# Performance work log

Hardware: AMD Instinct MI355X
Metric: run time of the kernel (lower is better)

Reference implementation:

```python
import jax, jax.numpy as jnp
import numpy as np

N = 50000      # nodes
E = 800000     # edges (before self-loops)
IN = 128       # in_channels
HID = 32       # hidden_channels
H = 4          # heads (hidden layers)
H_LAST = 6     # heads of final conv (concat=False -> mean)
OUT = 2        # out_channels
NEG = 0.2      # LeakyReLU slope in GATConv


def setup_inputs() -> dict:
    key = jax.random.key(0)
    ks = jax.random.split(key, 24)
    r = lambda k, s, sc=0.1: (jax.random.normal(k, s, jnp.float32) * sc)
    inp = {
        "x": jax.random.normal(ks[0], (N, IN), jnp.float32),
        "edge_index": jax.random.randint(ks[1], (2, E), 0, N, dtype=jnp.int32),
        "edge_attr": jax.random.normal(ks[2], (E, 1), jnp.float32),  # ignored by GATConv (edge_dim=None)
        # layer 0: GATConv(IN -> HID, heads=H, concat) + Linear(IN -> HID*H)
        "c0_W": r(ks[3], (IN, H * HID)), "c0_as": r(ks[4], (H, HID)), "c0_ad": r(ks[5], (H, HID)), "c0_b": jnp.zeros((H * HID,), jnp.float32),
        "l0_W": r(ks[6], (IN, H * HID)), "l0_b": jnp.zeros((H * HID,), jnp.float32),
        # layer 1 (middle): GATConv(HID*H -> HID, heads=H) + Linear(HID*H -> HID*H)
        "c1_W": r(ks[7], (H * HID, H * HID)), "c1_as": r(ks[8], (H, HID)), "c1_ad": r(ks[9], (H, HID)), "c1_b": jnp.zeros((H * HID,), jnp.float32),
        "l1_W": r(ks[10], (H * HID, H * HID)), "l1_b": jnp.zeros((H * HID,), jnp.float32),
        # layer 2 (last): GATConv(HID*H -> OUT, heads=H_LAST, concat=False) + Linear(HID*H -> OUT)
        "c2_W": r(ks[11], (H * HID, H_LAST * OUT)), "c2_as": r(ks[12], (H_LAST, OUT)), "c2_ad": r(ks[13], (H_LAST, OUT)), "c2_b": jnp.zeros((OUT,), jnp.float32),
        "l2_W": r(ks[14], (H * HID, OUT)), "l2_b": jnp.zeros((OUT,), jnp.float32),
    }
    return inp


def gat_conv(x, src, dst, W, a_src, a_dst, b, heads, ch, concat):
    n = x.shape[0]
    xw = (x @ W).reshape(n, heads, ch)                      # [N,H,C]
    al_s = jnp.einsum('nhc,hc->nh', xw, a_src)              # [N,H]
    al_d = jnp.einsum('nhc,hc->nh', xw, a_dst)
    alpha = jax.nn.leaky_relu(al_s[src] + al_d[dst], NEG)   # [E,H]
    # segment softmax over edges sharing the same destination node
    m = jax.ops.segment_max(alpha, dst, num_segments=n)
    e = jnp.exp(alpha - m[dst])
    s = jax.ops.segment_sum(e, dst, num_segments=n)
    coef = e / s[dst]                                       # [E,H]
    out = jax.ops.segment_sum(xw[src] * coef[:, :, None], dst, num_segments=n)  # [N,H,C]
    out = out.reshape(n, heads * ch) if concat else out.mean(axis=1)
    return out + b


def reference(x, edge_index, edge_attr,
              c0_W, c0_as, c0_ad, c0_b, l0_W, l0_b,
              c1_W, c1_as, c1_ad, c1_b, l1_W, l1_b,
              c2_W, c2_as, c2_ad, c2_b, l2_W, l2_b):
    n = x.shape[0]
    loops = jnp.arange(n, dtype=edge_index.dtype)  # GATConv add_self_loops=True
    src = jnp.concatenate([edge_index[0], loops])
    dst = jnp.concatenate([edge_index[1], loops])
    # edge_attr is ignored: GATConv built without edge_dim has lin_edge=None
    h = jax.nn.relu(gat_conv(x, src, dst, c0_W, c0_as, c0_ad, c0_b, H, HID, True) + x @ l0_W + l0_b)
    h = jax.nn.relu(gat_conv(h, src, dst, c1_W, c1_as, c1_ad, c1_b, H, HID, True) + h @ l1_W + l1_b)
    out = gat_conv(h, src, dst, c2_W, c2_as, c2_ad, c2_b, H_LAST, OUT, False) + h @ l2_W + l2_b
    return out
```

## Files before the change

kernel.cpp:

```cpp
#include <hip/hip_runtime.h>
#include <hip/hip_bf16.h>


#define NEG_SLOPE 0.2f
#define SC_CHUNK 4096
#define CAP 64
#define XCROWS 16

typedef __attribute__((ext_vector_type(8))) short short8;
typedef __attribute__((ext_vector_type(4))) float floatx4;

static __device__ __forceinline__ float leaky(float x) {
    return x > 0.f ? x : NEG_SLOPE * x;
}

static __device__ __forceinline__ unsigned short f2bf(float f) {
    unsigned int u = __float_as_uint(f);
    u = (u + 0x7fffu + ((u >> 16) & 1u)) >> 16;
    return (unsigned short)u;
}

static __device__ __forceinline__ unsigned int pack_bf2(float lo, float hi) {
    return (unsigned int)f2bf(lo) | ((unsigned int)f2bf(hi) << 16);
}

static __device__ __forceinline__ float bflo(unsigned int u) {
    return __uint_as_float(u << 16);
}
static __device__ __forceinline__ float bfhi(unsigned int u) {
    return __uint_as_float(u & 0xffff0000u);
}

__global__ __launch_bounds__(256) void k_bucket(
    const int* __restrict__ ei, int E, int N, int rs, int chunks,
    int* __restrict__ cnt, unsigned short* __restrict__ col,
    const float* __restrict__ W0, unsigned short* __restrict__ T0,
    const float* __restrict__ W1, unsigned short* __restrict__ T1,
    const float* __restrict__ W2, unsigned short* __restrict__ T2,
    const float* __restrict__ W3, unsigned short* __restrict__ T3,
    const float* __restrict__ c2W, const float* __restrict__ l2W,
    unsigned short* __restrict__ WT5,
    const float* __restrict__ x, unsigned short* __restrict__ Ab0, int Mpad) {
    int y = blockIdx.y;
    if (y == chunks) {
        int tid = blockIdx.x * 256 + threadIdx.x;
        for (int j = tid; j < 65536; j += 2048) {
            int wsel = j >> 14, t = j & 16383;
            int n = t >> 7, k = t & 127;
            const float* W = (wsel == 0) ? W0 : (wsel == 1) ? W1 : (wsel == 2) ? W2 : W3;
            unsigned short* T = (wsel == 0) ? T0 : (wsel == 1) ? T1 : (wsel == 2) ? T2 : T3;
            T[n * 128 + k] = f2bf(W[k * 128 + n]);
        }
        {
            int n = tid >> 7, k = tid & 127;
            float v = 0.f;
            if (n < 12) v = c2W[k * 12 + n];
            else if (n < 14) v = l2W[k * 2 + (n - 12)];
            WT5[n * 128 + k] = f2bf(v);
        }
        return;
    }
    if (y > chunks) {
        int bid = (y - chunks - 1) * 8 + blockIdx.x;
        int tid = bid * 256 + threadIdx.x;
        int total = Mpad * 32;
        int nvalid = N * 32;
        const float4* x4 = (const float4*)x;
        ushort4* o4 = (ushort4*)Ab0;
        for (int i = tid; i < total; i += XCROWS * 8 * 256) {
            ushort4 o;
            if (i < nvalid) {
                float4 v = x4[i];
                o.x = f2bf(v.x); o.y = f2bf(v.y);
                o.z = f2bf(v.z); o.w = f2bf(v.w);
            } else {
                o.x = 0; o.y = 0; o.z = 0; o.w = 0;
            }
            o4[i] = o;
        }
        return;
    }
    int lo = blockIdx.x * rs, hi = lo + rs;
    int base = y * SC_CHUNK;
    int ET = E + N;
#pragma unroll 4
    for (int o = threadIdx.x; o < SC_CHUNK; o += 256) {
        int e = base + o;
        if (e >= ET) break;
        int d = (e < E) ? ei[E + e] : (e - E);
        if (d < lo || d >= hi) continue;
        int s = (e < E) ? ei[e] : d;
        int pos = atomicAdd(&cnt[d], 1);
        if (pos < CAP) col[(d << 6) + pos] = (unsigned short)s;
    }
}

__global__ __launch_bounds__(256) void k_gemm2(
    const unsigned short* __restrict__ Ab,
    const unsigned short* __restrict__ WcT,
    const unsigned short* __restrict__ WlT,
    unsigned int* __restrict__ XWb,
    const float* __restrict__ a_s, const float* __restrict__ a_d,
    float4* __restrict__ ALS4, float4* __restrict__ ALD4,
    const float* __restrict__ lb,
    unsigned short* __restrict__ Hsb,
    int M) {
    __shared__ short8 Wl[128 * 17];
    int w = threadIdx.x >> 6, lane = threadIdx.x & 63;
    int m = lane & 15, q = lane >> 4;
    const short8* A8 = (const short8*)Ab;

    for (int u = threadIdx.x; u < 2048; u += 256)
        Wl[(u >> 4) * 17 + (u & 15)] = ((const short8*)WcT)[u];

    short8 af[2][4];
    int rt0 = blockIdx.x * 8 + w;
#pragma unroll
    for (int t = 0; t < 2; t++) {
        int arow = (rt0 + t * 4) * 16 + m;
#pragma unroll
        for (int ks = 0; ks < 4; ks++)
            af[t][ks] = A8[arow * 16 + ks * 4 + q];
    }
    __syncthreads();

#pragma unroll
    for (int t = 0; t < 2; t++) {
        floatx4 acc[8];
#pragma unroll
        for (int ct = 0; ct < 8; ct++) acc[ct] = (floatx4){0.f, 0.f, 0.f, 0.f};
#pragma unroll
        for (int ks = 0; ks < 4; ks++) {
#pragma unroll
            for (int ct = 0; ct < 8; ct++) {
                short8 bfrag = Wl[(ct * 16 + m) * 17 + ks * 4 + q];
                acc[ct] = __builtin_amdgcn_mfma_f32_16x16x32_bf16(af[t][ks], bfrag, acc[ct], 0, 0, 0);
            }
        }
        int crow0 = (rt0 + t * 4) * 16 + q * 4;
#pragma unroll
        for (int ct = 0; ct < 4; ct++) {
#pragma unroll
            for (int r = 0; r < 4; r++) {
                int gr = crow0 + r;
                if (gr < M)
                    XWb[gr * 64 + ct * 16 + m] = pack_bf2(acc[ct][r], acc[ct + 4][r]);
            }
        }
        float sv[4][4], dv[4][4];
#pragma unroll
        for (int h = 0; h < 4; h++) {
            float as0 = a_s[h * 32 + m], as1 = a_s[h * 32 + 16 + m];
            float ad0 = a_d[h * 32 + m], ad1 = a_d[h * 32 + 16 + m];
#pragma unroll
            for (int r = 0; r < 4; r++) {
                sv[h][r] = acc[2 * h][r] * as0 + acc[2 * h + 1][r] * as1;
                dv[h][r] = acc[2 * h][r] * ad0 + acc[2 * h + 1][r] * ad1;
            }
        }
#pragma unroll
        for (int off = 8; off >= 1; off >>= 1) {
#pragma unroll
            for (int h = 0; h < 4; h++)
#pragma unroll
                for (int r = 0; r < 4; r++) {
                    sv[h][r] += __shfl_xor(sv[h][r], off);
                    dv[h][r] += __shfl_xor(dv[h][r], off);
                }
        }
        if (m == 0) {
#pragma unroll
            for (int r = 0; r < 4; r++) {
                int gr = crow0 + r;
                if (gr < M) {
                    ALS4[gr] = make_float4(sv[0][r], sv[1][r], sv[2][r], sv[3][r]);
                    ALD4[gr] = make_float4(dv[0][r], dv[1][r], dv[2][r], dv[3][r]);
                }
            }
        }
    }

    __syncthreads();
    for (int u = threadIdx.x; u < 2048; u += 256)
        Wl[(u >> 4) * 17 + (u & 15)] = ((const short8*)WlT)[u];
    __syncthreads();

#pragma unroll
    for (int t = 0; t < 2; t++) {
        floatx4 acc[8];
#pragma unroll
        for (int ct = 0; ct < 8; ct++) acc[ct] = (floatx4){0.f, 0.f, 0.f, 0.f};
#pragma unroll
        for (int ks = 0; ks < 4; ks++) {
#pragma unroll
            for (int ct = 0; ct < 8; ct++) {
                short8 bfrag = Wl[(ct * 16 + m) * 17 + ks * 4 + q];
                acc[ct] = __builtin_amdgcn_mfma_f32_16x16x32_bf16(af[t][ks], bfrag, acc[ct], 0, 0, 0);
            }
        }
        int crow0 = (rt0 + t * 4) * 16 + q * 4;
#pragma unroll
        for (int ct = 0; ct < 8; ct++) {
            int gc = ct * 16 + m;
            float bias = lb[gc];
#pragma unroll
            for (int r = 0; r < 4; r++) {
                int gr = crow0 + r;
                if (gr < M) Hsb[gr * 128 + gc] = f2bf(acc[ct][r] + bias);
            }
        }
    }
}

__global__ __launch_bounds__(256) void k_gemm_small(
    const unsigned short* __restrict__ Ab,
    const unsigned short* __restrict__ WT5,
    const float* __restrict__ c2as, const float* __restrict__ c2ad,
    const float* __restrict__ l2b,
    float* __restrict__ L2D, float* __restrict__ ALD2,
    float* __restrict__ out, int M) {
    int w = threadIdx.x >> 6, lane = threadIdx.x & 63;
    int m = lane & 15, q = lane >> 4;
    const short8* A8 = (const short8*)Ab;
    const short8* W8 = (const short8*)WT5;
    floatx4 acc = (floatx4){0.f, 0.f, 0.f, 0.f};
    int arow = blockIdx.x * 64 + w * 16 + m;
#pragma unroll
    for (int ks = 0; ks < 4; ks++) {
        short8 afrag = A8[arow * 16 + ks * 4 + q];
        short8 bfrag = W8[m * 16 + ks * 4 + q];
        acc = __builtin_amdgcn_mfma_f32_16x16x32_bf16(afrag, bfrag, acc, 0, 0, 0);
    }
    float asm_ = (m < 12) ? c2as[m] : 0.f;
    float adm  = (m < 12) ? c2ad[m] : 0.f;
    int crow0 = blockIdx.x * 64 + w * 16 + q * 4;
    float sc[4], dc[4];
#pragma unroll
    for (int r = 0; r < 4; r++) {
        sc[r] = acc[r] * asm_;
        dc[r] = acc[r] * adm;
    }
#pragma unroll
    for (int r = 0; r < 4; r++) {
        sc[r] += __shfl_xor(sc[r], 1);
        dc[r] += __shfl_xor(dc[r], 1);
    }
#pragma unroll
    for (int r = 0; r < 4; r++) {
        int gr = crow0 + r;
        if (gr >= M) continue;
        if (m < 12) {
            L2D[gr * 20 + m] = acc[r];
            if ((m & 1) == 0) {
                int h = m >> 1;
                L2D[gr * 20 + 12 + h] = sc[r];
                ALD2[gr * 8 + h] = dc[r];
            }
        } else if (m == 12) {
            out[gr * 2 + 0] = acc[r] + l2b[0];
        } else if (m == 13) {
            out[gr * 2 + 1] = acc[r] + l2b[1];
        }
    }
}

__global__ __launch_bounds__(256) void k_agg4(
    const int* __restrict__ cntv, const unsigned short* __restrict__ col,
    const uint4* __restrict__ XWb4,
    const float4* __restrict__ ALS4, const float4* __restrict__ ALD4,
    const float* __restrict__ cb,
    const unsigned short* __restrict__ Hsb, unsigned short* __restrict__ Hb, int N) {
    int wid = threadIdx.x >> 6, lane = threadIdx.x & 63;
    int node = blockIdx.x * 4 + wid;
    if (node >= N) return;
    int deg = cntv[node];
    if (deg > CAP) deg = CAP;
    int start = node << 6;
    int gq = lane >> 4, g = lane & 15;
    int hA = g >> 3;
    int cval = col[start + lane];
    float4 cl = ((const float4*)cb)[g];
    float4 ch = ((const float4*)cb)[g + 16];
    uint2 skl = ((const uint2*)(Hsb + node * 128))[g];
    uint2 skh = ((const uint2*)(Hsb + node * 128 + 64))[g];
    float4 ad = ALD4[node];
    float adA = hA ? ad.y : ad.x;
    float adB = hA ? ad.w : ad.z;

    float a0 = 0.f, a1 = 0.f, a2 = 0.f, a3 = 0.f;
    float b0 = 0.f, b1 = 0.f, b2 = 0.f, b3 = 0.f;
    float sA = 0.f, sB = 0.f;

#define QUAD(qq)                                                        \
    bool t##qq; float4 as##qq; uint4 u##qq;                             \
    {                                                                   \
        int idx = (qq) * 4 + gq;                                        \
        t##qq = idx < deg;                                              \
        int sv = __shfl(cval, t##qq ? idx : 0);                         \
        as##qq = ALS4[sv];                                              \
        u##qq = XWb4[(size_t)sv * 16 + g];                              \
    }

#define CQ(qq)                                                          \
    {                                                                   \
        float eA = t##qq ? __expf(leaky((hA ? as##qq.y : as##qq.x) + adA)) : 0.f; \
        float eB = t##qq ? __expf(leaky((hA ? as##qq.w : as##qq.z) + adB)) : 0.f; \
        sA += eA; sB += eB;                                             \
        a0 += eA * bflo(u##qq.x); b0 += eB * bfhi(u##qq.x);             \
        a1 += eA * bflo(u##qq.y); b1 += eB * bfhi(u##qq.y);             \
        a2 += eA * bflo(u##qq.z); b2 += eB * bfhi(u##qq.z);             \
        a3 += eA * bflo(u##qq.w); b3 += eB * bfhi(u##qq.w);             \
    }

    if (deg <= 16) {
        QUAD(0) QUAD(1) QUAD(2) QUAD(3)
        CQ(0) CQ(1) CQ(2) CQ(3)
    } else if (deg <= 24) {
        QUAD(0) QUAD(1) QUAD(2) QUAD(3) QUAD(4) QUAD(5)
        CQ(0) CQ(1) CQ(2) CQ(3) CQ(4) CQ(5)
    } else {
        QUAD(0) QUAD(1) QUAD(2) QUAD(3) QUAD(4) QUAD(5) QUAD(6) QUAD(7)
        CQ(0) CQ(1) CQ(2) CQ(3) CQ(4) CQ(5) CQ(6) CQ(7)
        for (int i = 32; i < deg; i += 4) {
            int idx = i + gq;
            bool tt = idx < deg;
            int sv = __shfl(cval, tt ? idx : 0);
            float4 as = ALS4[sv];
            uint4 uu = XWb4[(size_t)sv * 16 + g];
            float eA = tt ? __expf(leaky((hA ? as.y : as.x) + adA)) : 0.f;
            float eB = tt ? __expf(leaky((hA ? as.w : as.z) + adB)) : 0.f;
            sA += eA; sB += eB;
            a0 += eA * bflo(uu.x); b0 += eB * bfhi(uu.x);
            a1 += eA * bflo(uu.y); b1 += eB * bfhi(uu.y);
            a2 += eA * bflo(uu.z); b2 += eB * bfhi(uu.z);
            a3 += eA * bflo(uu.w); b3 += eB * bfhi(uu.w);
        }
    }
#undef QUAD
#undef CQ

#define RED2(v) { v += __shfl_xor(v, 16); v += __shfl_xor(v, 32); }
    RED2(sA) RED2(sB)
    RED2(a0) RED2(a1) RED2(a2) RED2(a3)
    RED2(b0) RED2(b1) RED2(b2) RED2(b3)
#undef RED2

    if (gq == 0) {
        float invA = 1.f / sA, invB = 1.f / sB;
        float v0 = a0 * invA + cl.x + bflo(skl.x);
        float v1 = a1 * invA + cl.y + bfhi(skl.x);
        float v2 = a2 * invA + cl.z + bflo(skl.y);
        float v3 = a3 * invA + cl.w + bfhi(skl.y);
        float w0 = b0 * invB + ch.x + bflo(skh.x);
        float w1 = b1 * invB + ch.y + bfhi(skh.x);
        float w2 = b2 * invB + ch.z + bflo(skh.y);
        float w3 = b3 * invB + ch.w + bfhi(skh.y);
        v0 = v0 > 0.f ? v0 : 0.f;  v1 = v1 > 0.f ? v1 : 0.f;
        v2 = v2 > 0.f ? v2 : 0.f;  v3 = v3 > 0.f ? v3 : 0.f;
        w0 = w0 > 0.f ? w0 : 0.f;  w1 = w1 > 0.f ? w1 : 0.f;
        w2 = w2 > 0.f ? w2 : 0.f;  w3 = w3 > 0.f ? w3 : 0.f;
        uint2 ol, oh;
        ol.x = pack_bf2(v0, v1); ol.y = pack_bf2(v2, v3);
        oh.x = pack_bf2(w0, w1); oh.y = pack_bf2(w2, w3);
        ((uint2*)(Hb + node * 128))[g] = ol;
        ((uint2*)(Hb + node * 128 + 64))[g] = oh;
    }
}

__global__ __launch_bounds__(256) void k_agg2(
    const int* __restrict__ cntv, const unsigned short* __restrict__ col,
    const float4* __restrict__ L2D4,
    const float* __restrict__ ALD2,
    const float* __restrict__ c2b,
    float* __restrict__ out, int N) {
    int g = threadIdx.x >> 4, l = threadIdx.x & 15;
    int node = blockIdx.x * 16 + g;
    if (node >= N) return;
    int deg = cntv[node];
    if (deg > CAP) deg = CAP;
    int start = node << 6;

    float m0 = (l      < deg) ? 1.f : 0.f;
    float m1 = (l + 16 < deg) ? 1.f : 0.f;
    float m2 = (l + 32 < deg) ? 1.f : 0.f;
    float m3 = (l + 48 < deg) ? 1.f : 0.f;
    int s0 = col[start + ((l      < deg) ? l      : 0)];
    int s1 = col[start + ((l + 16 < deg) ? l + 16 : 0)];
    int s2 = col[start + ((l + 32 < deg) ? l + 32 : 0)];
    int s3 = col[start + ((l + 48 < deg) ? l + 48 : 0)];

    float ald[6];
    {
        float4 d03 = *(const float4*)(ALD2 + node * 8);
        float2 d45 = *(const float2*)(ALD2 + node * 8 + 4);
        ald[0] = d03.x; ald[1] = d03.y; ald[2] = d03.z; ald[3] = d03.w;
        ald[4] = d45.x; ald[5] = d45.y;
    }

#define LOADN(k, sv)                                                       \
    float4 xA##k = L2D4[(size_t)(sv) * 5 + 0];                             \
    float4 xB##k = L2D4[(size_t)(sv) * 5 + 1];                             \
    float4 xC##k = L2D4[(size_t)(sv) * 5 + 2];                             \
    float4 aS##k = L2D4[(size_t)(sv) * 5 + 3];                             \
    float4 aT##k = L2D4[(size_t)(sv) * 5 + 4];
    LOADN(0, s0) LOADN(1, s1) LOADN(2, s2) LOADN(3, s3)
#undef LOADN

    float se[6], a0[6], a1[6];
#pragma unroll
    for (int h = 0; h < 6; h++) { se[h] = 0.f; a0[h] = 0.f; a1[h] = 0.f; }

#define COMPN(k, mk)                                                       \
    {                                                                      \
        float als[6] = {aS##k.x, aS##k.y, aS##k.z, aS##k.w, aT##k.x, aT##k.y}; \
        float xw[12] = {xA##k.x, xA##k.y, xA##k.z, xA##k.w,                \
                        xB##k.x, xB##k.y, xB##k.z, xB##k.w,                \
                        xC##k.x, xC##k.y, xC##k.z, xC##k.w};               \
        _Pragma("unroll")                                                  \
        for (int h = 0; h < 6; h++) {                                      \
            float e = (mk) * __expf(leaky(als[h] + ald[h]));               \
            se[h] += e;                                                    \
            a0[h] += e * xw[2 * h];                                        \
            a1[h] += e * xw[2 * h + 1];                                    \
        }                                                                  \
    }
    COMPN(0, m0) COMPN(1, m1) COMPN(2, m2) COMPN(3, m3)
#undef COMPN

#pragma unroll
    for (int m = 8; m >= 1; m >>= 1) {
#pragma unroll
        for (int h = 0; h < 6; h++) {
            se[h] += __shfl_xor(se[h], m);
            a0[h] += __shfl_xor(a0[h], m);
            a1[h] += __shfl_xor(a1[h], m);
        }
    }
    if (l == 0) {
        float o0 = 0.f, o1 = 0.f;
#pragma unroll
        for (int h = 0; h < 6; h++) {
            float inv = 1.f / se[h];
            o0 += a0[h] * inv;
            o1 += a1[h] * inv;
        }
        out[node * 2 + 0] += o0 * (1.f / 6.f) + c2b[0];
        out[node * 2 + 1] += o1 * (1.f / 6.f) + c2b[1];
    }
}


extern "C" void kernel_launch(void* const* d_in, const int* in_sizes, int n_in,
                              void* d_out, int out_size, void* d_ws, size_t ws_size,
                              hipStream_t stream) {
    const float* x   = (const float*)d_in[0];
    const int* ei    = (const int*)d_in[1];
    const float* c0W = (const float*)d_in[3];
    const float* c0as = (const float*)d_in[4];
    const float* c0ad = (const float*)d_in[5];
    const float* c0b = (const float*)d_in[6];
    const float* l0W = (const float*)d_in[7];
    const float* l0b = (const float*)d_in[8];
    const float* c1W = (const float*)d_in[9];
    const float* c1as = (const float*)d_in[10];
    const float* c1ad = (const float*)d_in[11];
    const float* c1b = (const float*)d_in[12];
    const float* l1W = (const float*)d_in[13];
    const float* l1b = (const float*)d_in[14];
    const float* c2W = (const float*)d_in[15];
    const float* c2as = (const float*)d_in[16];
    const float* c2ad = (const float*)d_in[17];
    const float* c2b = (const float*)d_in[18];
    const float* l2W = (const float*)d_in[19];
    const float* l2b = (const float*)d_in[20];
    float* out = (float*)d_out;

    const int N = in_sizes[0] / 128;
    const int E = in_sizes[1] / 2;
    const int ET = E + N;
    const int Mpad = (N + 63) & ~63;

    char* p = (char*)d_ws;
    auto alloc = [&](size_t bytes) -> void* {
        void* r = (void*)p;
        p += (bytes + 255) & ~(size_t)255;
        return r;
    };
    unsigned short* Hsb = (unsigned short*)alloc((size_t)N * 128 * 2);
    unsigned int* XWb  = (unsigned int*)alloc((size_t)N * 64 * 4);
    unsigned short* Ab0 = (unsigned short*)alloc((size_t)Mpad * 128 * 2);
    unsigned short* AbH = (unsigned short*)alloc((size_t)Mpad * 128 * 2);
    unsigned short* W1T = (unsigned short*)alloc(128 * 128 * 2);
    unsigned short* W2T = (unsigned short*)alloc(128 * 128 * 2);
    unsigned short* W3T = (unsigned short*)alloc(128 * 128 * 2);
    unsigned short* W4T = (unsigned short*)alloc(128 * 128 * 2);
    unsigned short* WT5 = (unsigned short*)alloc(16 * 128 * 2);
    float* ALS = (float*)alloc((size_t)N * 4 * 4);
    float* ALD = (float*)alloc((size_t)N * 8 * 4);
    float* L2D = (float*)alloc((size_t)N * 20 * 4);
    int* cnt    = (int*)alloc((size_t)N * 4);
    unsigned short* col = (unsigned short*)alloc((size_t)N * CAP * 2);

    hipMemsetAsync(cnt, 0, (size_t)N * 4, stream);
    int rs = (N + 7) / 8;
    int chunks = (ET + SC_CHUNK - 1) / SC_CHUNK;
    dim3 bgrid(8, chunks + 1 + XCROWS);
    k_bucket<<<bgrid, 256, 0, stream>>>(ei, E, N, rs, chunks, cnt, col,
                                        c0W, W1T, l0W, W2T, c1W, W3T, l1W, W4T,
                                        c2W, l2W, WT5, x, Ab0, Mpad);

    int gx = (Mpad + 127) / 128;
    int nwb = (N + 3) / 4;

    k_gemm2<<<gx, 256, 0, stream>>>(Ab0, W1T, W2T, XWb, c0as, c0ad,
                                    (float4*)ALS, (float4*)ALD, l0b, Hsb, N);
    k_agg4<<<nwb, 256, 0, stream>>>(cnt, col, (const uint4*)XWb,
                                    (const float4*)ALS, (const float4*)ALD,
                                    c0b, Hsb, AbH, N);

    k_gemm2<<<gx, 256, 0, stream>>>(AbH, W3T, W4T, XWb, c1as, c1ad,
                                    (float4*)ALS, (float4*)ALD, l1b, Hsb, N);
    k_agg4<<<nwb, 256, 0, stream>>>(cnt, col, (const uint4*)XWb,
                                    (const float4*)ALS, (const float4*)ALD,
                                    c1b, Hsb, Ab0, N);

    k_gemm_small<<<Mpad / 64, 256, 0, stream>>>(Ab0, WT5, c2as, c2ad, l2b,
                                                L2D, ALD, out, N);
    k_agg2<<<(N + 15) / 16, 256, 0, stream>>>(cnt, col, (const float4*)L2D,
                                              ALD, c2b, out, N);
}
```

Measured before the change: 297.5 us.

## Fuse final small GEMM into layer-1 aggregation kernel

Merges the last-layer projection (128->14 GEMM plus the attention logits) into the second aggregation kernel. The projection becomes an FP32 dot product against weights staged in shared memory, followed by a shuffle reduction. This removes one kernel launch and the round trip of the bf16 hidden activations through global memory. In exchange, every block rebuilds the weight table in LDS and runs extra shuffles, and the separate per-layer ALD buffers are split so the two layers no longer alias.

Result: slower. 308.3 us (+3.6%).

```diff
diff --git a/kernel.cpp b/kernel.cpp
--- a/kernel.cpp
+++ b/kernel.cpp
@@ -208,58 +208,6 @@
                 int gr = crow0 + r;
                 if (gr < M) Hsb[gr * 128 + gc] = f2bf(acc[ct][r] + bias);
             }
-        }
-    }
-}
-
-__global__ __launch_bounds__(256) void k_gemm_small(
-    const unsigned short* __restrict__ Ab,
-    const unsigned short* __restrict__ WT5,
-    const float* __restrict__ c2as, const float* __restrict__ c2ad,
-    const float* __restrict__ l2b,
-    float* __restrict__ L2D, float* __restrict__ ALD2,
-    float* __restrict__ out, int M) {
-    int w = threadIdx.x >> 6, lane = threadIdx.x & 63;
-    int m = lane & 15, q = lane >> 4;
-    const short8* A8 = (const short8*)Ab;
-    const short8* W8 = (const short8*)WT5;
-    floatx4 acc = (floatx4){0.f, 0.f, 0.f, 0.f};
-    int arow = blockIdx.x * 64 + w * 16 + m;
-#pragma unroll
-    for (int ks = 0; ks < 4; ks++) {
-        short8 afrag = A8[arow * 16 + ks * 4 + q];
-        short8 bfrag = W8[m * 16 + ks * 4 + q];
-        acc = __builtin_amdgcn_mfma_f32_16x16x32_bf16(afrag, bfrag, acc, 0, 0, 0);
-    }
-    float asm_ = (m < 12) ? c2as[m] : 0.f;
-    float adm  = (m < 12) ? c2ad[m] : 0.f;
-    int crow0 = blockIdx.x * 64 + w * 16 + q * 4;
-    float sc[4], dc[4];
-#pragma unroll
-    for (int r = 0; r < 4; r++) {
-        sc[r] = acc[r] * asm_;
-        dc[r] = acc[r] * adm;
-    }
-#pragma unroll
-    for (int r = 0; r < 4; r++) {
-        sc[r] += __shfl_xor(sc[r], 1);
-        dc[r] += __shfl_xor(dc[r], 1);
-    }
-#pragma unroll
-    for (int r = 0; r < 4; r++) {
-        int gr = crow0 + r;
-        if (gr >= M) continue;
-        if (m < 12) {
-            L2D[gr * 20 + m] = acc[r];
-            if ((m & 1) == 0) {
-                int h = m >> 1;
-                L2D[gr * 20 + 12 + h] = sc[r];
-                ALD2[gr * 8 + h] = dc[r];
-            }
-        } else if (m == 12) {
-            out[gr * 2 + 0] = acc[r] + l2b[0];
-        } else if (m == 13) {
-            out[gr * 2 + 1] = acc[r] + l2b[1];
         }
     }
 }
@@ -367,6 +315,149 @@
     }
 }
 
+__global__ __launch_bounds__(256) void k_agg4f(
+    const int* __restrict__ cntv, const unsigned short* __restrict__ col,
+    const uint4* __restrict__ XWb4,
+    const float4* __restrict__ ALS4, const float4* __restrict__ ALD4,
+    const float* __restrict__ cb,
+    const unsigned short* __restrict__ Hsb,
+    const unsigned short* __restrict__ WT5,
+    const float* __restrict__ c2as, const float* __restrict__ c2ad,
+    const float* __restrict__ l2b,
+    float* __restrict__ L2D, float* __restrict__ AL2D,
+    float* __restrict__ out, int N) {
+    __shared__ float Wf[16 * 132];
+    for (int t = threadIdx.x; t < 2048; t += 256) {
+        int n = t >> 7, k = t & 127;
+        Wf[n * 132 + k] = __uint_as_float(((unsigned int)WT5[t]) << 16);
+    }
+    __syncthreads();
+
+    int wid = threadIdx.x >> 6, lane = threadIdx.x & 63;
+    int node = blockIdx.x * 4 + wid;
+    if (node >= N) return;
+    int deg = cntv[node];
+    if (deg > CAP) deg = CAP;
+    int start = node << 6;
+    int gq = lane >> 4, g = lane & 15;
+    int hA = g >> 3;
+    int cval = col[start + lane];
+    float4 cl = ((const float4*)cb)[g];
+    float4 ch = ((const float4*)cb)[g + 16];
+    uint2 skl = ((const uint2*)(Hsb + node * 128))[g];
+    uint2 skh = ((const uint2*)(Hsb + node * 128 + 64))[g];
+    float4 ad = ALD4[node];
+    float adA = hA ? ad.y : ad.x;
+    float adB = hA ? ad.w : ad.z;
+
+    float a0 = 0.f, a1 = 0.f, a2 = 0.f, a3 = 0.f;
+    float b0 = 0.f, b1 = 0.f, b2 = 0.f, b3 = 0.f;
+    float sA = 0.f, sB = 0.f;
+
+#define QUAD(qq)                                                        \
+    bool t##qq; float4 as##qq; uint4 u##qq;                             \
+    {                                                                   \
+        int idx = (qq) * 4 + gq;                                        \
+        t##qq = idx < deg;                                              \
+        int sv = __shfl(cval, t##qq ? idx : 0);                         \
+        as##qq = ALS4[sv];                                              \
+        u##qq = XWb4[(size_t)sv * 16 + g];                              \
+    }
+
+#define CQ(qq)                                                          \
+    {                                                                   \
+        float eA = t##qq ? __expf(leaky((hA ? as##qq.y : as##qq.x) + adA)) : 0.f; \
+        float eB = t##qq ? __expf(leaky((hA ? as##qq.w : as##qq.z) + adB)) : 0.f; \
+        sA += eA; sB += eB;                                             \
+        a0 += eA * bflo(u##qq.x); b0 += eB * bfhi(u##qq.x);             \
+        a1 += eA * bflo(u##qq.y); b1 += eB * bfhi(u##qq.y);             \
+        a2 += eA * bflo(u##qq.z); b2 += eB * bfhi(u##qq.z);             \
+        a3 += eA * bflo(u##qq.w); b3 += eB * bfhi(u##qq.w);             \
+    }
+
+    if (deg <= 16) {
+        QUAD(0) QUAD(1) QUAD(2) QUAD(3)
+        CQ(0) CQ(1) CQ(2) CQ(3)
+    } else if (deg <= 24) {
+        QUAD(0) QUAD(1) QUAD(2) QUAD(3) QUAD(4) QUAD(5)
+        CQ(0) CQ(1) CQ(2) CQ(3) CQ(4) CQ(5)
+    } else {
+        QUAD(0) QUAD(1) QUAD(2) QUAD(3) QUAD(4) QUAD(5) QUAD(6) QUAD(7)
+        CQ(0) CQ(1) CQ(2) CQ(3) CQ(4) CQ(5) CQ(6) CQ(7)
+        for (int i = 32; i < deg; i += 4) {
+            int idx = i + gq;
+            bool tt = idx < deg;
+            int sv = __shfl(cval, tt ? idx : 0);
+            float4 as = ALS4[sv];
+            uint4 uu = XWb4[(size_t)sv * 16 + g];
+            float eA = tt ? __expf(leaky((hA ? as.y : as.x) + adA)) : 0.f;
+            float eB = tt ? __expf(leaky((hA ? as.w : as.z) + adB)) : 0.f;
+            sA += eA; sB += eB;
+            a0 += eA * bflo(uu.x); b0 += eB * bfhi(uu.x);
+            a1 += eA * bflo(uu.y); b1 += eB * bfhi(uu.y);
+            a2 += eA * bflo(uu.z); b2 += eB * bfhi(uu.z);
+            a3 += eA * bflo(uu.w); b3 += eB * bfhi(uu.w);
+        }
+    }
+#undef QUAD
+#undef CQ
+
+#define RED2(v) { v += __shfl_xor(v, 16); v += __shfl_xor(v, 32); }
+    RED2(sA) RED2(sB)
+    RED2(a0) RED2(a1) RED2(a2) RED2(a3)
+    RED2(b0) RED2(b1) RED2(b2) RED2(b3)
+#undef RED2
+
+    float invA = 1.f / sA, invB = 1.f / sB;
+    float v0 = a0 * invA + cl.x + bflo(skl.x);
+    float v1 = a1 * invA + cl.y + bfhi(skl.x);
+    float v2 = a2 * invA + cl.z + bflo(skl.y);
+    float v3 = a3 * invA + cl.w + bfhi(skl.y);
+    float w0 = b0 * invB + ch.x + bflo(skh.x);
+    float w1 = b1 * invB + ch.y + bfhi(skh.x);
+    float w2 = b2 * invB + ch.z + bflo(skh.y);
+    float w3 = b3 * invB + ch.w + bfhi(skh.y);
+    v0 = v0 > 0.f ? v0 : 0.f;  v1 = v1 > 0.f ? v1 : 0.f;
+    v2 = v2 > 0.f ? v2 : 0.f;  v3 = v3 > 0.f ? v3 : 0.f;
+    w0 = w0 > 0.f ? w0 : 0.f;  w1 = w1 > 0.f ? w1 : 0.f;
+    w2 = w2 > 0.f ? w2 : 0.f;  w3 = w3 > 0.f ? w3 : 0.f;
+    unsigned pl0 = pack_bf2(v0, v1), pl1 = pack_bf2(v2, v3);
+    unsigned ph0 = pack_bf2(w0, w1), ph1 = pack_bf2(w2, w3);
+    float rv0 = bflo(pl0), rv1 = bfhi(pl0), rv2 = bflo(pl1), rv3 = bfhi(pl1);
+    float rw0 = bflo(ph0), rw1 = bfhi(ph0), rw2 = bflo(ph1), rw3 = bfhi(ph1);
+
+    float part[4];
+#pragma unroll
+    for (int j = 0; j < 4; j++) {
+        int n = (gq << 2) + j;
+        const float* wr = Wf + n * 132;
+        float4 wa = *(const float4*)(wr + 4 * g);
+        float4 wb = *(const float4*)(wr + 64 + 4 * g);
+        part[j] = rv0 * wa.x + rv1 * wa.y + rv2 * wa.z + rv3 * wa.w
+                + rw0 * wb.x + rw1 * wb.y + rw2 * wb.z + rw3 * wb.w;
+    }
+#pragma unroll
+    for (int mm = 1; mm <= 8; mm <<= 1) {
+#pragma unroll
+        for (int j = 0; j < 4; j++) part[j] += __shfl_xor(part[j], mm);
+    }
+    if (g < 4) {
+        int n = (gq << 2) + g;
+        float val = part[g];
+        if (n < 12) L2D[node * 20 + n] = val;
+        else if (n == 12) out[node * 2 + 0] = val + l2b[0];
+        else if (n == 13) out[node * 2 + 1] = val + l2b[1];
+    }
+    if (gq < 3 && (g == 4 || g == 5)) {
+        int j0 = (g - 4) * 2;
+        int n0 = (gq << 2) + j0;
+        int h = n0 >> 1;
+        float o0 = part[j0], o1 = part[j0 + 1];
+        L2D[node * 20 + 12 + h] = o0 * c2as[n0] + o1 * c2as[n0 + 1];
+        AL2D[node * 8 + h]      = o0 * c2ad[n0] + o1 * c2ad[n0 + 1];
+    }
+}
+
 __global__ __launch_bounds__(256) void k_agg2(
     const int* __restrict__ cntv, const unsigned short* __restrict__ col,
     const float4* __restrict__ L2D4,
@@ -420,7 +511,7 @@
         for (int h = 0; h < 6; h++) {                                      \
             float e = (mk) * __expf(leaky(als[h] + ald[h]));               \
             se[h] += e;                                                    \
-            a0[h] += e * xw[2 * h];                                        \
+            a0[h] += e * xw[2 * h];                                       \
             a1[h] += e * xw[2 * h + 1];                                    \
         }                                                                  \
     }
@@ -496,7 +587,8 @@
     unsigned short* W4T = (unsigned short*)alloc(128 * 128 * 2);
     unsigned short* WT5 = (unsigned short*)alloc(16 * 128 * 2);
     float* ALS = (float*)alloc((size_t)N * 4 * 4);
-    float* ALD = (float*)alloc((size_t)N * 8 * 4);
+    float* ALD = (float*)alloc((size_t)N * 4 * 4);
+    float* AL2D = (float*)alloc((size_t)N * 8 * 4);
     float* L2D = (float*)alloc((size_t)N * 20 * 4);
     int* cnt    = (int*)alloc((size_t)N * 4);
     unsigned short* col = (unsigned short*)alloc((size_t)N * CAP * 2);
@@ -520,12 +612,11 @@
 
     k_gemm2<<<gx, 256, 0, stream>>>(AbH, W3T, W4T, XWb, c1as, c1ad,
                                     (float4*)ALS, (float4*)ALD, l1b, Hsb, N);
-    k_agg4<<<nwb, 256, 0, stream>>>(cnt, col, (const uint4*)XWb,
-                                    (const float4*)ALS, (const float4*)ALD,
-                                    c1b, Hsb, Ab0, N);
-
-    k_gemm_small<<<Mpad / 64, 256, 0, stream>>>(Ab0, WT5, c2as, c2ad, l2b,
-                                                L2D, ALD, out, N);
+    k_agg4f<<<nwb, 256, 0, stream>>>(cnt, col, (const uint4*)XWb,
+                                     (const float4*)ALS, (const float4*)ALD,
+                                     c1b, Hsb, WT5, c2as, c2ad, l2b,
+                                     L2D, AL2D, out, N);
+
     k_agg2<<<(N + 15) / 16, 256, 0, stream>>>(cnt, col, (const float4*)L2D,
-                                              ALD, c2b, out, N);
-}
+                                              AL2D, c2b, out, N);
+}
```
